# Kernel tuning notes

Hardware: AMD Instinct MI355X
Metric: run time of the kernel (lower is better)

The kernel has to match this reference:

```python
import jax, jax.numpy as jnp
import numpy as np


def _gcs_conv(x, a, w1, w2, b):
    # GCSConv: relu(A @ x W1 + x W2 + b);  x:[B,N,F], a:[B,N,N]
    return jax.nn.relu(jnp.einsum('bij,bjh->bih', a, x @ w1) + x @ w2 + b)


def _topk_pool(x, a, p, ratio=0.5):
    # score y = x . p/||p||, keep top ceil(ratio*N) nodes per graph,
    # gate kept node features with sigmoid(y), slice adjacency rows+cols.
    y = x @ (p / jnp.linalg.norm(p))            # [B, N]
    k = int(np.ceil(ratio * y.shape[1]))
    yk, idx = jax.lax.top_k(y, k)               # [B, k]
    xk = jnp.take_along_axis(x, idx[:, :, None], axis=1)
    xk = xk * jax.nn.sigmoid(yk)[:, :, None]    # gated node features [B,k,H]
    ak = jnp.take_along_axis(a, idx[:, :, None], axis=1)
    ak = jnp.take_along_axis(ak, idx[:, None, :], axis=2)  # [B,k,k]
    return xk, ak


def setup_inputs() -> dict:
    B, N, F0, H, C = 256, 512, 128, 32, 16
    key = jax.random.key(0)
    ks = jax.random.split(key, 12)
    s = lambda fan: 1.0 / np.sqrt(fan)
    return {
        'x': jax.random.normal(ks[0], (B, N, F0), jnp.float32),
        'a': jax.random.uniform(ks[1], (B, N, N), jnp.float32),
        'w1_1': jax.random.normal(ks[2], (F0, H), jnp.float32) * s(F0),
        'w2_1': jax.random.normal(ks[3], (F0, H), jnp.float32) * s(F0),
        'b1': jnp.zeros((H,), jnp.float32),
        'w1_2': jax.random.normal(ks[4], (H, H), jnp.float32) * s(H),
        'w2_2': jax.random.normal(ks[5], (H, H), jnp.float32) * s(H),
        'b2': jnp.zeros((H,), jnp.float32),
        'w1_3': jax.random.normal(ks[6], (H, H), jnp.float32) * s(H),
        'w2_3': jax.random.normal(ks[7], (H, H), jnp.float32) * s(H),
        'b3': jnp.zeros((H,), jnp.float32),
        'p_pool': jax.random.normal(ks[8], (H,), jnp.float32),
        'wd': jax.random.normal(ks[9], (H, C), jnp.float32) * s(H),
        'bd': jnp.zeros((C,), jnp.float32),
    }


def reference(x, a, w1_1, w2_1, b1, w1_2, w2_2, b2, w1_3, w2_3, b3, p_pool, wd, bd):
    x = _gcs_conv(x, a, w1_1, w2_1, b1)
    # NOTE: original code reuses pool1 twice -> shared p_pool for both stages
    x1, a1 = _topk_pool(x, a, p_pool)
    x1 = _gcs_conv(x1, a1, w1_2, w2_2, b2)
    x2, a2 = _topk_pool(x1, a1, p_pool)
    x2 = _gcs_conv(x2, a2, w1_3, w2_3, b3)
    pooled = jnp.mean(x2, axis=1)               # GlobalAvgPool over nodes [B,H]
    return jax.nn.softmax(pooled @ wd + bd, axis=-1)
```

## Files before the change

### kernel.cpp

```cpp
#include <hip/hip_runtime.h>
#include <cmath>

#define B 256
#define N0 512
#define F0 128
#define H 32
#define NC 16

template<int F, int RPT, int NPB, bool SCATTER>
__global__ __launch_bounds__(256) void k_xw(
    const float* __restrict__ x, const float* __restrict__ w1,
    const float* __restrict__ w2, const float* __restrict__ bias,
    const int* __restrict__ sidx,
    float* __restrict__ h, float* __restrict__ g) {
  __shared__ float w1t[H][F + 4];
  __shared__ float w2t[H][F + 4];
  __shared__ float bs[H];
  const int tid = threadIdx.x;
  for (int i = tid; i < F * H; i += 256) {
    int f = i >> 5, hc = i & 31;
    w1t[hc][f] = w1[i];
    w2t[hc][f] = w2[i];
  }
  if (tid < H) bs[tid] = bias[tid];
  __syncthreads();
  const int hq = tid & 7;
  const int rq = tid >> 3;
  const size_t row0 = (size_t)blockIdx.x * (32 * RPT) + (size_t)rq * RPT;
  const float* xb = x + row0 * F;
  float acc1[RPT][4];
  float acc2[RPT][4];
  #pragma unroll
  for (int r = 0; r < RPT; ++r)
    for (int c = 0; c < 4; ++c) { acc1[r][c] = 0.f; acc2[r][c] = 0.f; }
  for (int f0 = 0; f0 < F; f0 += 4) {
    float4 w1v[4], w2v[4];
    #pragma unroll
    for (int hh = 0; hh < 4; ++hh) {
      w1v[hh] = *(const float4*)&w1t[hq * 4 + hh][f0];
      w2v[hh] = *(const float4*)&w2t[hq * 4 + hh][f0];
    }
    #pragma unroll
    for (int r = 0; r < RPT; ++r) {
      float4 xv = *(const float4*)(xb + (size_t)r * F + f0);
      #pragma unroll
      for (int hh = 0; hh < 4; ++hh) {
        acc1[r][hh] += xv.x * w1v[hh].x + xv.y * w1v[hh].y + xv.z * w1v[hh].z + xv.w * w1v[hh].w;
        acc2[r][hh] += xv.x * w2v[hh].x + xv.y * w2v[hh].y + xv.z * w2v[hh].z + xv.w * w2v[hh].w;
      }
    }
  }
  #pragma unroll
  for (int r = 0; r < RPT; ++r) {
    size_t row = row0 + r;
    size_t go = row * H + hq * 4;
    size_t ho;
    if (SCATTER) {
      int b = (int)(row / NPB);
      int gid = sidx[row];
      ho = ((size_t)b * N0 + gid) * H + hq * 4;
    } else {
      ho = go;
    }
    float4 hv = make_float4(acc1[r][0], acc1[r][1], acc1[r][2], acc1[r][3]);
    float4 gv = make_float4(acc2[r][0] + bs[hq * 4 + 0], acc2[r][1] + bs[hq * 4 + 1],
                            acc2[r][2] + bs[hq * 4 + 2], acc2[r][3] + bs[hq * 4 + 3]);
    *(float4*)(h + ho) = hv;
    *(float4*)(g + go) = gv;
  }
}

template<int NROW, int RPT>
__global__ __launch_bounds__(256) void k_amm(
    const float* __restrict__ a0, const int* __restrict__ rid,
    const float* __restrict__ hf, const float* __restrict__ gbuf,
    float* __restrict__ out) {
  constexpr int JC = 128;
  __shared__ float hs[JC * H];
  const int tid = threadIdx.x;
  const int b = blockIdx.x;
  const int hq = tid & 7;
  const int rq = tid >> 3;
  const int row0 = blockIdx.y * (32 * RPT) + rq * RPT;
  const float* arow[RPT];
  #pragma unroll
  for (int r = 0; r < RPT; ++r) {
    int row = row0 + r;
    int grow = rid ? rid[(size_t)b * NROW + row] : row;
    arow[r] = a0 + ((size_t)b * N0 + grow) * N0;
  }
  float acc[RPT][4];
  #pragma unroll
  for (int r = 0; r < RPT; ++r) { acc[r][0] = acc[r][1] = acc[r][2] = acc[r][3] = 0.f; }
  for (int j0 = 0; j0 < N0; j0 += JC) {
    __syncthreads();
    const float4* src = (const float4*)(hf + ((size_t)b * N0 + j0) * H);
    float4* dst = (float4*)hs;
    #pragma unroll
    for (int i = 0; i < JC * H / 4 / 256; ++i) dst[tid + i * 256] = src[tid + i * 256];
    __syncthreads();
    #pragma unroll 4
    for (int j = 0; j < JC; j += 4) {
      float4 hv[4];
      #pragma unroll
      for (int jj = 0; jj < 4; ++jj) hv[jj] = *(const float4*)&hs[(j + jj) * H + hq * 4];
      #pragma unroll
      for (int r = 0; r < RPT; ++r) {
        float4 av = *(const float4*)(arow[r] + j0 + j);
        acc[r][0] += av.x * hv[0].x + av.y * hv[1].x + av.z * hv[2].x + av.w * hv[3].x;
        acc[r][1] += av.x * hv[0].y + av.y * hv[1].y + av.z * hv[2].y + av.w * hv[3].y;
        acc[r][2] += av.x * hv[0].z + av.y * hv[1].z + av.z * hv[2].z + av.w * hv[3].z;
        acc[r][3] += av.x * hv[0].w + av.y * hv[1].w + av.z * hv[2].w + av.w * hv[3].w;
      }
    }
  }
  #pragma unroll
  for (int r = 0; r < RPT; ++r) {
    int row = row0 + r;
    size_t o = ((size_t)b * NROW + row) * H + hq * 4;
    float4 gv = *(const float4*)(gbuf + o);
    float4 ov = make_float4(fmaxf(acc[r][0] + gv.x, 0.f), fmaxf(acc[r][1] + gv.y, 0.f),
                            fmaxf(acc[r][2] + gv.z, 0.f), fmaxf(acc[r][3] + gv.w, 0.f));
    *(float4*)(out + o) = ov;
  }
}

__global__ __launch_bounds__(256) void k_zero(float4* __restrict__ p, int n4) {
  int i = blockIdx.x * 256 + threadIdx.x;
  if (i < n4) p[i] = make_float4(0.f, 0.f, 0.f, 0.f);
}

template<int NN, int K>
__global__ __launch_bounds__(256) void k_topk(
    const float* __restrict__ x, const float* __restrict__ p,
    const int* __restrict__ prev_idx,
    float* __restrict__ xg, int* __restrict__ out_idx) {
  __shared__ float ys[NN];
  __shared__ int is[NN];
  __shared__ float ps[H];
  __shared__ float pns;
  const int tid = threadIdx.x;
  const int b = blockIdx.x;
  if (tid < H) ps[tid] = p[tid];
  __syncthreads();
  if (tid == 0) {
    float s = 0.f;
    for (int i = 0; i < H; ++i) s += ps[i] * ps[i];
    pns = 1.f / sqrtf(s);
  }
  __syncthreads();
  for (int i = tid; i < NN; i += 256) {
    const float* xr = x + ((size_t)b * NN + i) * H;
    float s = 0.f;
    #pragma unroll
    for (int f = 0; f < H; ++f) s += xr[f] * ps[f];
    ys[i] = s * pns;
    is[i] = i;
  }
  for (int k = 2; k <= NN; k <<= 1) {
    for (int j = k >> 1; j > 0; j >>= 1) {
      __syncthreads();
      for (int i = tid; i < NN; i += 256) {
        int ixj = i ^ j;
        if (ixj > i) {
          float v0 = ys[i], v1 = ys[ixj];
          int i0 = is[i], i1 = is[ixj];
          bool pre = (v1 > v0) || (v1 == v0 && i1 < i0);
          bool doswap = ((i & k) == 0) ? pre : !pre;
          if (doswap) { ys[i] = v1; ys[ixj] = v0; is[i] = i1; is[ixj] = i0; }
        }
      }
    }
  }
  for (int k = 2; k <= K; k <<= 1) {
    for (int j = k >> 1; j > 0; j >>= 1) {
      __syncthreads();
      for (int i = tid; i < K; i += 256) {
        int ixj = i ^ j;
        if (ixj > i && ixj < K) {
          float v0 = ys[i], v1 = ys[ixj];
          int i0 = is[i], i1 = is[ixj];
          bool pre = (i1 < i0);
          bool doswap = ((i & k) == 0) ? pre : !pre;
          if (doswap) { ys[i] = v1; ys[ixj] = v0; is[i] = i1; is[ixj] = i0; }
        }
      }
    }
  }
  __syncthreads();
  for (int t = tid; t < K * H; t += 256) {
    int kk = t >> 5, f = t & 31;
    int loc = is[kk];
    float gate = 1.f / (1.f + expf(-ys[kk]));
    xg[((size_t)b * K + kk) * H + f] = x[((size_t)b * NN + loc) * H + f] * gate;
  }
  for (int t = tid; t < K; t += 256)
    out_idx[(size_t)b * K + t] = prev_idx ? prev_idx[(size_t)b * NN + is[t]] : is[t];
}

__global__ __launch_bounds__(128) void k_head(
    const float* __restrict__ xl3, const float* __restrict__ wd,
    const float* __restrict__ bd, float* __restrict__ out) {
  __shared__ float part[4][H];
  __shared__ float pooled[H];
  __shared__ float wds[H * NC];
  __shared__ float logits[NC];
  const int tid = threadIdx.x;
  const int b = blockIdx.x;
  for (int i = tid; i < H * NC; i += 128) wds[i] = wd[i];
  const int f = tid & 31, nq = tid >> 5;
  float s = 0.f;
  for (int n = nq * 32; n < nq * 32 + 32; ++n)
    s += xl3[((size_t)b * 128 + n) * H + f];
  part[nq][f] = s;
  __syncthreads();
  if (tid < H)
    pooled[tid] = (part[0][tid] + part[1][tid] + part[2][tid] + part[3][tid]) * (1.f / 128.f);
  __syncthreads();
  if (tid < NC) {
    float acc = bd[tid];
    for (int i = 0; i < H; ++i) acc += pooled[i] * wds[i * NC + tid];
    logits[tid] = acc;
  }
  __syncthreads();
  if (tid == 0) {
    float mx = logits[0];
    for (int i = 1; i < NC; ++i) mx = fmaxf(mx, logits[i]);
    float e[NC], se = 0.f;
    for (int i = 0; i < NC; ++i) { e[i] = expf(logits[i] - mx); se += e[i]; }
    float inv = 1.f / se;
    for (int i = 0; i < NC; ++i) out[(size_t)b * NC + i] = e[i] * inv;
  }
}

extern "C" void kernel_launch(void* const* d_in, const int* in_sizes, int n_in,
                              void* d_out, int out_size, void* d_ws, size_t ws_size,
                              hipStream_t stream) {
  (void)in_sizes; (void)n_in; (void)out_size; (void)ws_size;
  const float* x    = (const float*)d_in[0];
  const float* a    = (const float*)d_in[1];
  const float* w1_1 = (const float*)d_in[2];
  const float* w2_1 = (const float*)d_in[3];
  const float* b1   = (const float*)d_in[4];
  const float* w1_2 = (const float*)d_in[5];
  const float* w2_2 = (const float*)d_in[6];
  const float* b2   = (const float*)d_in[7];
  const float* w1_3 = (const float*)d_in[8];
  const float* w2_3 = (const float*)d_in[9];
  const float* b3   = (const float*)d_in[10];
  const float* pp   = (const float*)d_in[11];
  const float* wd   = (const float*)d_in[12];
  const float* bd   = (const float*)d_in[13];
  float* out = (float*)d_out;

  char* w = (char*)d_ws;
  auto take = [&](size_t bytes) { char* r = w; w += (bytes + 255) & ~(size_t)255; return r; };
  float* h1  = (float*)take((size_t)B * N0 * H * 4);
  float* g1  = (float*)take((size_t)B * N0 * H * 4);
  float* xl1 = (float*)take((size_t)B * N0 * H * 4);
  int*   id1 = (int*)  take((size_t)B * 256 * 4);
  float* xg1 = (float*)take((size_t)B * 256 * H * 4);
  float* g2  = (float*)take((size_t)B * 256 * H * 4);
  float* xl2 = (float*)take((size_t)B * 256 * H * 4);
  int*   id2 = (int*)  take((size_t)B * 128 * 4);
  float* xg2 = (float*)take((size_t)B * 128 * H * 4);
  float* g3  = (float*)take((size_t)B * 128 * H * 4);
  float* xl3 = (float*)take((size_t)B * 128 * H * 4);
  float* hf2 = h1;
  float* hf3 = g1;

  k_xw<F0, 4, N0, false><<<dim3(B * N0 / 128), dim3(256), 0, stream>>>(
      x, w1_1, w2_1, b1, nullptr, h1, g1);
  k_amm<512, 2><<<dim3(B, 8), dim3(256), 0, stream>>>(a, nullptr, h1, g1, xl1);
  k_zero<<<dim3(2 * B * N0 * H / 4 / 256), dim3(256), 0, stream>>>(
      (float4*)h1, 2 * B * N0 * H / 4);
  k_topk<512, 256><<<dim3(B), dim3(256), 0, stream>>>(xl1, pp, nullptr, xg1, id1);
  k_xw<H, 4, 256, true><<<dim3(B * 256 / 128), dim3(256), 0, stream>>>(
      xg1, w1_2, w2_2, b2, id1, hf2, g2);
  k_amm<256, 2><<<dim3(B, 4), dim3(256), 0, stream>>>(a, id1, hf2, g2, xl2);
  k_topk<256, 128><<<dim3(B), dim3(256), 0, stream>>>(xl2, pp, id1, xg2, id2);
  k_xw<H, 4, 128, true><<<dim3(B * 128 / 128), dim3(256), 0, stream>>>(
      xg2, w1_3, w2_3, b3, id2, hf3, g3);
  k_amm<128, 1><<<dim3(B, 4), dim3(256), 0, stream>>>(a, id2, hf3, g3, xl3);
  k_head<<<dim3(B), dim3(128), 0, stream>>>(xl3, wd, bd, out);
}
```

Baseline: 676.0 us.

## Stage adjacency tiles through shared memory with coalesced loads in k_amm

The aggregation kernel now loads a tile of adjacency rows into shared memory cooperatively, with each group of 16 threads reading one row chunk contiguously, instead of each thread streaming its own rows directly from global memory with strided per-thread accesses. Row indices are resolved once into shared memory, and the column chunk drops to 64 with a padded stride to limit bank conflicts. The first layer also doubles rows per thread and halves the grid. This adds shared-memory traffic and a barrier per chunk in exchange for better coalescing of the dominant adjacency reads.

```diff
diff --git a/kernel.cpp b/kernel.cpp
--- a/kernel.cpp
+++ b/kernel.cpp
@@ -75,48 +75,62 @@
     const float* __restrict__ a0, const int* __restrict__ rid,
     const float* __restrict__ hf, const float* __restrict__ gbuf,
     float* __restrict__ out) {
-  constexpr int JC = 128;
-  __shared__ float hs[JC * H];
+  constexpr int RB = 32 * RPT;
+  constexpr int JC = 64;
+  constexpr int AS = JC + 2;
+  __shared__ float atile[RB][AS];
+  __shared__ float htile[JC][H];
+  __shared__ int rowid[RB];
   const int tid = threadIdx.x;
   const int b = blockIdx.x;
+  const int row0 = blockIdx.y * RB;
+  for (int i = tid; i < RB; i += 256) {
+    int row = row0 + i;
+    rowid[i] = rid ? rid[(size_t)b * NROW + row] : row;
+  }
+  __syncthreads();
   const int hq = tid & 7;
   const int rq = tid >> 3;
-  const int row0 = blockIdx.y * (32 * RPT) + rq * RPT;
-  const float* arow[RPT];
-  #pragma unroll
-  for (int r = 0; r < RPT; ++r) {
-    int row = row0 + r;
-    int grow = rid ? rid[(size_t)b * NROW + row] : row;
-    arow[r] = a0 + ((size_t)b * N0 + grow) * N0;
-  }
+  const float* abase = a0 + (size_t)b * N0 * N0;
   float acc[RPT][4];
   #pragma unroll
   for (int r = 0; r < RPT; ++r) { acc[r][0] = acc[r][1] = acc[r][2] = acc[r][3] = 0.f; }
   for (int j0 = 0; j0 < N0; j0 += JC) {
-    __syncthreads();
-    const float4* src = (const float4*)(hf + ((size_t)b * N0 + j0) * H);
-    float4* dst = (float4*)hs;
+    if (j0) __syncthreads();
+    {
+      const float4* src = (const float4*)(hf + ((size_t)b * N0 + j0) * H);
+      float4* dst = (float4*)htile;
+      #pragma unroll
+      for (int i = 0; i < JC * H / 4 / 256; ++i) dst[tid + i * 256] = src[tid + i * 256];
+    }
     #pragma unroll
-    for (int i = 0; i < JC * H / 4 / 256; ++i) dst[tid + i * 256] = src[tid + i * 256];
+    for (int i = 0; i < RB * 16 / 256; ++i) {
+      int c = tid + i * 256;
+      int r = c >> 4, jc = c & 15;
+      float4 v = *(const float4*)(abase + (size_t)rowid[r] * N0 + j0 + jc * 4);
+      *(float2*)&atile[r][jc * 4] = make_float2(v.x, v.y);
+      *(float2*)&atile[r][jc * 4 + 2] = make_float2(v.z, v.w);
+    }
     __syncthreads();
     #pragma unroll 4
     for (int j = 0; j < JC; j += 4) {
       float4 hv[4];
       #pragma unroll
-      for (int jj = 0; jj < 4; ++jj) hv[jj] = *(const float4*)&hs[(j + jj) * H + hq * 4];
+      for (int jj = 0; jj < 4; ++jj) hv[jj] = *(const float4*)&htile[j + jj][hq * 4];
       #pragma unroll
       for (int r = 0; r < RPT; ++r) {
-        float4 av = *(const float4*)(arow[r] + j0 + j);
-        acc[r][0] += av.x * hv[0].x + av.y * hv[1].x + av.z * hv[2].x + av.w * hv[3].x;
-        acc[r][1] += av.x * hv[0].y + av.y * hv[1].y + av.z * hv[2].y + av.w * hv[3].y;
-        acc[r][2] += av.x * hv[0].z + av.y * hv[1].z + av.z * hv[2].z + av.w * hv[3].z;
-        acc[r][3] += av.x * hv[0].w + av.y * hv[1].w + av.z * hv[2].w + av.w * hv[3].w;
+        float2 a01 = *(const float2*)&atile[rq * RPT + r][j];
+        float2 a23 = *(const float2*)&atile[rq * RPT + r][j + 2];
+        acc[r][0] += a01.x * hv[0].x + a01.y * hv[1].x + a23.x * hv[2].x + a23.y * hv[3].x;
+        acc[r][1] += a01.x * hv[0].y + a01.y * hv[1].y + a23.x * hv[2].y + a23.y * hv[3].y;
+        acc[r][2] += a01.x * hv[0].z + a01.y * hv[1].z + a23.x * hv[2].z + a23.y * hv[3].z;
+        acc[r][3] += a01.x * hv[0].w + a01.y * hv[1].w + a23.x * hv[2].w + a23.y * hv[3].w;
       }
     }
   }
   #pragma unroll
   for (int r = 0; r < RPT; ++r) {
-    int row = row0 + r;
+    int row = row0 + rq * RPT + r;
     size_t o = ((size_t)b * NROW + row) * H + hq * 4;
     float4 gv = *(const float4*)(gbuf + o);
     float4 ov = make_float4(fmaxf(acc[r][0] + gv.x, 0.f), fmaxf(acc[r][1] + gv.y, 0.f),
@@ -271,7 +285,7 @@
 
   k_xw<F0, 4, N0, false><<<dim3(B * N0 / 128), dim3(256), 0, stream>>>(
       x, w1_1, w2_1, b1, nullptr, h1, g1);
-  k_amm<512, 2><<<dim3(B, 8), dim3(256), 0, stream>>>(a, nullptr, h1, g1, xl1);
+  k_amm<512, 4><<<dim3(B, 4), dim3(256), 0, stream>>>(a, nullptr, h1, g1, xl1);
   k_zero<<<dim3(2 * B * N0 * H / 4 / 256), dim3(256), 0, stream>>>(
       (float4*)h1, 2 * B * N0 * H / 4);
   k_topk<512, 256><<<dim3(B), dim3(256), 0, stream>>>(xl1, pp, nullptr, xg1, id1);
```

Result: faster. 639.2 us (-5.5%).
